# Performance work log

Hardware: AMD Instinct MI355X
Metric: run time of the kernel (lower is better)

The kernel has to match this reference:

```python
import jax, jax.numpy as jnp
import numpy as np

VOCAB, EMBED, HIDDEN = 128, 128, 256
BATCH, SEQ = 512, 512


def setup_inputs() -> dict:
    key = jax.random.key(0)
    ks = jax.random.split(key, 9)
    x = jax.random.randint(ks[0], (BATCH, SEQ), 0, VOCAB, dtype=jnp.int32)
    emb = jax.random.normal(ks[1], (VOCAB, EMBED), dtype=jnp.float32)
    s_hh = 1.0 / np.sqrt(HIDDEN)
    s_xh = 1.0 / np.sqrt(EMBED)
    s_hy = 1.0 / np.sqrt(HIDDEN)
    W_hh = jax.random.uniform(ks[2], (HIDDEN, HIDDEN), jnp.float32, -s_hh, s_hh)
    b_hh = jax.random.uniform(ks[3], (HIDDEN,), jnp.float32, -s_hh, s_hh)
    W_xh = jax.random.uniform(ks[4], (HIDDEN, EMBED), jnp.float32, -s_xh, s_xh)
    b_xh = jax.random.uniform(ks[5], (HIDDEN,), jnp.float32, -s_xh, s_xh)
    W_hy = jax.random.uniform(ks[6], (VOCAB, HIDDEN), jnp.float32, -s_hy, s_hy)
    b_hy = jax.random.uniform(ks[7], (VOCAB,), jnp.float32, -s_hy, s_hy)
    h0 = jax.random.normal(ks[8], (HIDDEN,), dtype=jnp.float32)
    return {"x": x, "emb": emb, "W_hh": W_hh, "b_hh": b_hh,
            "W_xh": W_xh, "b_xh": b_xh, "W_hy": W_hy, "b_hy": b_hy, "h0": h0}


def reference(x, emb, W_hh, b_hh, W_xh, b_xh, W_hy, b_hy, h0):
    xe = emb[x]                      # [B, S, E]
    B, S, E = xe.shape
    x0 = xe[:, 0]                    # first-token embedding, added every step (quirk in source)
    h_init = jnp.broadcast_to(h0, (B, h0.shape[0]))  # learned initial hidden, broadcast over batch

    def step(h, xt):
        h = jnp.tanh(h @ W_hh.T + b_hh + (xt + x0) @ W_xh.T + b_xh)
        y = h @ W_hy.T + b_hy        # [B, vocab]
        return h, y

    xs = jnp.swapaxes(xe[:, : S - 1], 0, 1)  # [S-1, B, E]
    _, ys = jax.lax.scan(step, h_init, xs)   # ys: [S-1, B, vocab]
    return jnp.swapaxes(ys, 0, 1)            # [B, S-1, vocab]
```

## Files before the change

kernel.cpp:

```cpp
#include <hip/hip_runtime.h>
#include <math.h>

namespace {
constexpr int SEQ   = 512;
constexpr int VOCAB = 128;
constexpr int EMBED = 128;
constexpr int HID   = 256;
constexpr int NSTEP = 511;
constexpr int BLK   = 512;
constexpr int NROW  = 2;
constexpr int NBLK  = 256;
}

__device__ float g_P[VOCAB * HID];

__global__ void precompute_P(const float* __restrict__ emb,
                             const float* __restrict__ Wxh)
{
    __shared__ __align__(16) float es[EMBED];
    const int v = blockIdx.x;
    const int j = threadIdx.x;
    if (j < EMBED) es[j] = emb[(size_t)v * EMBED + j];
    __syncthreads();
    const float4* w4 = (const float4*)(Wxh + (size_t)j * EMBED);
    const float4* e4 = (const float4*)es;
    float a = 0.f;
    #pragma unroll
    for (int k = 0; k < EMBED / 4; ++k) {
        float4 w = w4[k], e = e4[k];
        a += w.x * e.x + w.y * e.y + w.z * e.z + w.w * e.w;
    }
    g_P[v * HID + j] = a;
}

__device__ __forceinline__ int swz_c(int c) { return c ^ ((c >> 3) & 7); }

template<int WSTAG>
__global__ __launch_bounds__(BLK, 2)
void rnn_fused3(const int* __restrict__ x,   const float* __restrict__ Whh,
                const float* __restrict__ bhh, const float* __restrict__ bxh,
                const float* __restrict__ Why, const float* __restrict__ bhy,
                const float* __restrict__ h0,  float* __restrict__ out)
{
    __shared__ __align__(16) float h_s[2 * NROW * HID];

    const int tid = threadIdx.x;
    const int r0  = blockIdx.x * NROW;

    const int lk  = tid & 7;
    const int jg  = tid >> 3;
    const int jsel = (jg << 2) | (tid & 3);
    const int rsel = (tid & 4) ? 1 : 0;
    const int v0  = jg << 1;

    float whh[4][32];
    #pragma unroll
    for (int jj = 0; jj < 4; ++jj) {
        const float4* s4 = (const float4*)(Whh + (size_t)((jg << 2) + jj) * HID + (lk << 5));
        #pragma unroll
        for (int k4 = 0; k4 < 8; ++k4) {
            float4 f = s4[k4];
            whh[jj][4*k4+0] = f.x; whh[jj][4*k4+1] = f.y;
            whh[jj][4*k4+2] = f.z; whh[jj][4*k4+3] = f.w;
        }
    }
    float wy[2][32];
    #pragma unroll
    for (int r = 0; r < 2; ++r) {
        const float4* s4 = (const float4*)(Why + (size_t)(v0 + r) * HID + (lk << 5));
        #pragma unroll
        for (int k4 = 0; k4 < 8; ++k4) {
            float4 f = s4[k4];
            wy[r][4*k4+0] = f.x; wy[r][4*k4+1] = f.y;
            wy[r][4*k4+2] = f.z; wy[r][4*k4+3] = f.w;
        }
    }

    int hoff[8];
    #pragma unroll
    for (int i = 0; i < 8; ++i) hoff[i] = (lk << 7) + ((i ^ lk) << 4);

    int hwoff;
    {
        int c = jsel >> 2;
        hwoff = ((tid & 4) << 6) + ((swz_c(c) << 2) | (jsel & 3));
    }

    {
        int row = tid >> 8, j = tid & 255;
        h_s[row * HID + ((swz_c(j >> 2) << 2) | (j & 3))] = h0[j];
    }

    const size_t xb0 = (size_t)r0 * SEQ;
    const size_t xb1 = xb0 + SEQ;
    const int i00 = x[xb0];
    const int i01 = x[xb1];
    const int i0sel = rsel ? i01 : i00;
    const float pinit = g_P[(size_t)i0sel * HID + jsel];
    const float cst   = pinit + bhh[jsel] + bxh[jsel];
    float pt = pinit;
    int inx0 = x[xb0 + 1];
    int inx1 = x[xb1 + 1];

    const int orow = (lk >> 1) & 1;
    const int ov   = v0 + (lk & 1);
    float* outp = out + (size_t)(r0 + orow) * NSTEP * VOCAB + ov;
    const float bsel = bhy[ov];

    __syncthreads();

    for (int t = 0; t < NSTEP; ++t) {
        const int cur = t & 1, nxt = cur ^ 1;

        const int isel = rsel ? inx1 : inx0;
        const float pn = g_P[(size_t)isel * HID + jsel];
        {
            int tt = t + 2; tt = (tt < SEQ) ? tt : (SEQ - 1);
            inx0 = x[xb0 + tt];
            inx1 = x[xb1 + tt];
        }

        const char* hpar = (const char*)h_s + (cur << 11);
        float a0[4] = {0,0,0,0};
        float a1[4] = {0,0,0,0};
        #pragma unroll
        for (int i = 0; i < 8; ++i) {
            float4 h0v = *(const float4*)(hpar + hoff[i]);
            float4 h1v = *(const float4*)(hpar + 1024 + hoff[i]);
            #pragma unroll
            for (int jj = 0; jj < 4; ++jj) {
                a0[jj] += whh[jj][4*i+0]*h0v.x + whh[jj][4*i+1]*h0v.y
                        + whh[jj][4*i+2]*h0v.z + whh[jj][4*i+3]*h0v.w;
                a1[jj] += whh[jj][4*i+0]*h1v.x + whh[jj][4*i+1]*h1v.y
                        + whh[jj][4*i+2]*h1v.z + whh[jj][4*i+3]*h1v.w;
            }
        }
        float u0, u1;
        {
            float k0 = (lk & 1) ? a0[1] : a0[0];
            float s0 = (lk & 1) ? a0[0] : a0[1];
            k0 += __shfl_xor(s0, 1);
            float k1 = (lk & 1) ? a0[3] : a0[2];
            float s1 = (lk & 1) ? a0[2] : a0[3];
            k1 += __shfl_xor(s1, 1);
            float ka = (lk & 2) ? k1 : k0;
            float sa = (lk & 2) ? k0 : k1;
            ka += __shfl_xor(sa, 2);
            ka += __shfl_xor(ka, 4);
            u0 = ka;
        }
        {
            float k0 = (lk & 1) ? a1[1] : a1[0];
            float s0 = (lk & 1) ? a1[0] : a1[1];
            k0 += __shfl_xor(s0, 1);
            float k1 = (lk & 1) ? a1[3] : a1[2];
            float s1 = (lk & 1) ? a1[2] : a1[3];
            k1 += __shfl_xor(s1, 1);
            float ka = (lk & 2) ? k1 : k0;
            float sa = (lk & 2) ? k0 : k1;
            ka += __shfl_xor(sa, 2);
            ka += __shfl_xor(ka, 4);
            u1 = ka;
        }
        {
            float u = (rsel ? u1 : u0) + cst + pt;
            float e = __expf(2.0f * u);
            float hn = 1.0f - 2.0f / (e + 1.0f);
            h_s[(nxt << 9) + hwoff] = hn;
        }
        pt = pn;

        __syncthreads();

        {
            const char* hp = (const char*)h_s + (nxt << 11);
            float b00 = 0.f, b10 = 0.f, b01 = 0.f, b11 = 0.f;
            #pragma unroll
            for (int i = 0; i < 8; ++i) {
                float4 h0v = *(const float4*)(hp + hoff[i]);
                float4 h1v = *(const float4*)(hp + 1024 + hoff[i]);
                b00 += wy[0][4*i+0]*h0v.x + wy[0][4*i+1]*h0v.y
                     + wy[0][4*i+2]*h0v.z + wy[0][4*i+3]*h0v.w;
                b10 += wy[1][4*i+0]*h0v.x + wy[1][4*i+1]*h0v.y
                     + wy[1][4*i+2]*h0v.z + wy[1][4*i+3]*h0v.w;
                b01 += wy[0][4*i+0]*h1v.x + wy[0][4*i+1]*h1v.y
                     + wy[0][4*i+2]*h1v.z + wy[0][4*i+3]*h1v.w;
                b11 += wy[1][4*i+0]*h1v.x + wy[1][4*i+1]*h1v.y
                     + wy[1][4*i+2]*h1v.z + wy[1][4*i+3]*h1v.w;
            }
            float kr0 = (lk & 1) ? b10 : b00;
            float sr0 = (lk & 1) ? b00 : b10;
            kr0 += __shfl_xor(sr0, 1);
            float kr1 = (lk & 1) ? b11 : b01;
            float sr1 = (lk & 1) ? b01 : b11;
            kr1 += __shfl_xor(sr1, 1);
            float kv = (lk & 2) ? kr1 : kr0;
            float sv = (lk & 2) ? kr0 : kr1;
            kv += __shfl_xor(sv, 2);
            kv += __shfl_xor(kv, 4);
            if (lk < 4) *outp = kv + bsel;
            outp += VOCAB;
        }
    }
}

extern "C" void kernel_launch(void* const* d_in, const int* in_sizes, int n_in,
                              void* d_out, int out_size, void* d_ws, size_t ws_size,
                              hipStream_t stream)
{
    (void)in_sizes; (void)n_in; (void)d_ws; (void)out_size;
    const int*   x   = (const int*)  d_in[0];
    const float* emb = (const float*)d_in[1];
    const float* Whh = (const float*)d_in[2];
    const float* bhh = (const float*)d_in[3];
    const float* Wxh = (const float*)d_in[4];
    const float* bxh = (const float*)d_in[5];
    const float* Why = (const float*)d_in[6];
    const float* bhy = (const float*)d_in[7];
    const float* h0  = (const float*)d_in[8];
    float* out = (float*)d_out;

    precompute_P<<<VOCAB, 256, 0, stream>>>(emb, Wxh);

    const size_t needH  = (size_t)512 * 511 * 256 * 4;
    const size_t needHU = 2 * needH;
    if (ws_size >= needHU) {
        rnn_fused3<2><<<NBLK, BLK, 0, stream>>>(x, Whh, bhh, bxh, Why, bhy, h0, out);
    } else if (ws_size >= needH) {
        rnn_fused3<1><<<NBLK, BLK, 0, stream>>>(x, Whh, bhh, bxh, Why, bhy, h0, out);
    } else {
        rnn_fused3<0><<<NBLK, BLK, 0, stream>>>(x, Whh, bhh, bxh, Why, bhy, h0, out);
    }
}
```

Baseline: 1.076 ms.

## Move recurrent and output matmuls onto fp16 MFMA with hi/lo split

Replaces the scalar FP32 recurrence with MFMA 16x16x32 fp16 instructions. Each block now handles 16 batch rows with 4 waves instead of 2 rows with 512 threads. Both weights and hidden state are split into fp16 hi and lo parts, and three MFMAs per tile keep near-FP32 accuracy for the recurrent matmul. The output projection uses only the hi parts. Occupancy drops to 32 blocks on the device, and some precision is lost in the output projection, in exchange for far fewer FLOP instructions per step and fewer shuffle reductions.

```diff
diff --git a/kernel.cpp b/kernel.cpp
--- a/kernel.cpp
+++ b/kernel.cpp
@@ -1,5 +1,8 @@
 #include <hip/hip_runtime.h>
 #include <math.h>
+
+typedef _Float16 f16x8 __attribute__((ext_vector_type(8)));
+typedef float    f32x4 __attribute__((ext_vector_type(4)));
 
 namespace {
 constexpr int SEQ   = 512;
@@ -7,9 +10,11 @@
 constexpr int EMBED = 128;
 constexpr int HID   = 256;
 constexpr int NSTEP = 511;
-constexpr int BLK   = 512;
-constexpr int NROW  = 2;
-constexpr int NBLK  = 256;
+constexpr int BLK   = 256;
+constexpr int NROW  = 16;
+constexpr int NBLK  = 32;
+constexpr int NTA   = 4;
+constexpr int NTB   = 2;
 }
 
 __device__ float g_P[VOCAB * HID];
@@ -33,174 +38,170 @@
     g_P[v * HID + j] = a;
 }
 
-__device__ __forceinline__ int swz_c(int c) { return c ^ ((c >> 3) & 7); }
-
-template<int WSTAG>
-__global__ __launch_bounds__(BLK, 2)
-void rnn_fused3(const int* __restrict__ x,   const float* __restrict__ Whh,
-                const float* __restrict__ bhh, const float* __restrict__ bxh,
-                const float* __restrict__ Why, const float* __restrict__ bhy,
-                const float* __restrict__ h0,  float* __restrict__ out)
-{
-    __shared__ __align__(16) float h_s[2 * NROW * HID];
-
-    const int tid = threadIdx.x;
-    const int r0  = blockIdx.x * NROW;
-
-    const int lk  = tid & 7;
-    const int jg  = tid >> 3;
-    const int jsel = (jg << 2) | (tid & 3);
-    const int rsel = (tid & 4) ? 1 : 0;
-    const int v0  = jg << 1;
-
-    float whh[4][32];
-    #pragma unroll
-    for (int jj = 0; jj < 4; ++jj) {
-        const float4* s4 = (const float4*)(Whh + (size_t)((jg << 2) + jj) * HID + (lk << 5));
-        #pragma unroll
-        for (int k4 = 0; k4 < 8; ++k4) {
-            float4 f = s4[k4];
-            whh[jj][4*k4+0] = f.x; whh[jj][4*k4+1] = f.y;
-            whh[jj][4*k4+2] = f.z; whh[jj][4*k4+3] = f.w;
-        }
-    }
-    float wy[2][32];
-    #pragma unroll
-    for (int r = 0; r < 2; ++r) {
-        const float4* s4 = (const float4*)(Why + (size_t)(v0 + r) * HID + (lk << 5));
-        #pragma unroll
-        for (int k4 = 0; k4 < 8; ++k4) {
-            float4 f = s4[k4];
-            wy[r][4*k4+0] = f.x; wy[r][4*k4+1] = f.y;
-            wy[r][4*k4+2] = f.z; wy[r][4*k4+3] = f.w;
-        }
-    }
-
-    int hoff[8];
-    #pragma unroll
-    for (int i = 0; i < 8; ++i) hoff[i] = (lk << 7) + ((i ^ lk) << 4);
-
-    int hwoff;
+__device__ __forceinline__ void load_hilo(const float* s, f16x8& h8, f16x8& l8)
+{
+    float4 A = *(const float4*)s, B = *(const float4*)(s + 4);
+    _Float16 h;
+    h = (_Float16)A.x; h8[0] = h; l8[0] = (_Float16)(A.x - (float)h);
+    h = (_Float16)A.y; h8[1] = h; l8[1] = (_Float16)(A.y - (float)h);
+    h = (_Float16)A.z; h8[2] = h; l8[2] = (_Float16)(A.z - (float)h);
+    h = (_Float16)A.w; h8[3] = h; l8[3] = (_Float16)(A.w - (float)h);
+    h = (_Float16)B.x; h8[4] = h; l8[4] = (_Float16)(B.x - (float)h);
+    h = (_Float16)B.y; h8[5] = h; l8[5] = (_Float16)(B.y - (float)h);
+    h = (_Float16)B.z; h8[6] = h; l8[6] = (_Float16)(B.z - (float)h);
+    h = (_Float16)B.w; h8[7] = h; l8[7] = (_Float16)(B.w - (float)h);
+}
+
+
+__global__ __launch_bounds__(BLK, 1)
+void rnn_mfma5(const int* __restrict__ x,   const float* __restrict__ Whh,
+               const float* __restrict__ bhh, const float* __restrict__ bxh,
+               const float* __restrict__ Why, const float* __restrict__ bhy,
+               const float* __restrict__ h0,  float* __restrict__ out)
+{
+    __shared__ __align__(16) _Float16 hbuf_hi[2][NROW][HID];
+    __shared__ __align__(16) _Float16 hbuf_lo[2][NROW][HID];
+
+    const int tid  = threadIdx.x;
+    const int w    = tid >> 6;
+    const int lane = tid & 63;
+    const int ll   = lane & 15;
+    const int lh   = lane >> 4;
+    const int r0   = blockIdx.x * NROW;
+
+    f16x8 wa_hi[NTA][8], wa_lo[NTA][8];
+    #pragma unroll
+    for (int a = 0; a < NTA; ++a)
+        #pragma unroll
+        for (int f = 0; f < 8; ++f)
+            load_hilo(Whh + (size_t)(64 * w + 16 * a + ll) * HID + 32 * f + 8 * lh,
+                      wa_hi[a][f], wa_lo[a][f]);
+    f16x8 wy_hi[NTB][8];
+    #pragma unroll
+    for (int b = 0; b < NTB; ++b)
+        #pragma unroll
+        for (int f = 0; f < 8; ++f) {
+            f16x8 dummy_lo;
+            load_hilo(Why + (size_t)(32 * w + 16 * b + ll) * HID + 32 * f + 8 * lh,
+                      wy_hi[b][f], dummy_lo);
+        }
+
     {
-        int c = jsel >> 2;
-        hwoff = ((tid & 4) << 6) + ((swz_c(c) << 2) | (jsel & 3));
-    }
-
-    {
-        int row = tid >> 8, j = tid & 255;
-        h_s[row * HID + ((swz_c(j >> 2) << 2) | (j & 3))] = h0[j];
-    }
-
-    const size_t xb0 = (size_t)r0 * SEQ;
-    const size_t xb1 = xb0 + SEQ;
-    const int i00 = x[xb0];
-    const int i01 = x[xb1];
-    const int i0sel = rsel ? i01 : i00;
-    const float pinit = g_P[(size_t)i0sel * HID + jsel];
-    const float cst   = pinit + bhh[jsel] + bxh[jsel];
-    float pt = pinit;
-    int inx0 = x[xb0 + 1];
-    int inx1 = x[xb1 + 1];
-
-    const int orow = (lk >> 1) & 1;
-    const int ov   = v0 + (lk & 1);
-    float* outp = out + (size_t)(r0 + orow) * NSTEP * VOCAB + ov;
-    const float bsel = bhy[ov];
+        int k = tid;
+        float v = h0[k];
+        _Float16 hi = (_Float16)v;
+        _Float16 lo = (_Float16)(v - (float)hi);
+        int g = k >> 3, bb = k & 7;
+        #pragma unroll
+        for (int m = 0; m < NROW; ++m) {
+            int e = ((g ^ (m & 7)) << 3) + bb;
+            hbuf_hi[1][m][e] = hi;
+            hbuf_lo[1][m][e] = lo;
+        }
+    }
+
+    float cst[NTA][4], pt[NTA][4];
+    int   inx[4];
+    #pragma unroll
+    for (int r = 0; r < 4; ++r) {
+        const size_t xrow = (size_t)(r0 + 4 * lh + r) * SEQ;
+        int i0 = x[xrow];
+        #pragma unroll
+        for (int a = 0; a < NTA; ++a) {
+            int j = 64 * w + 16 * a + ll;
+            float p = g_P[(size_t)i0 * HID + j];
+            pt[a][r]  = p;
+            cst[a][r] = p + bhh[j] + bxh[j];
+        }
+        inx[r] = x[xrow + 1];
+    }
+    float bv[NTB];
+    #pragma unroll
+    for (int b = 0; b < NTB; ++b) bv[b] = bhy[32 * w + 16 * b + ll];
+
+    int aoff[8];
+    #pragma unroll
+    for (int f = 0; f < 8; ++f)
+        aoff[f] = 512 * ll + ((((f << 2) + lh) ^ (ll & 7)) << 4);
 
     __syncthreads();
 
+    f16x8 af_hi[8], af_lo[8];
+    #pragma unroll
+    for (int f = 0; f < 8; ++f) {
+        af_hi[f] = *(const f16x8*)((const char*)&hbuf_hi[1][0][0] + aoff[f]);
+        af_lo[f] = *(const f16x8*)((const char*)&hbuf_lo[1][0][0] + aoff[f]);
+    }
+
     for (int t = 0; t < NSTEP; ++t) {
-        const int cur = t & 1, nxt = cur ^ 1;
-
-        const int isel = rsel ? inx1 : inx0;
-        const float pn = g_P[(size_t)isel * HID + jsel];
+        f32x4 acc_hh[NTA] = {{0,0,0,0},{0,0,0,0},{0,0,0,0},{0,0,0,0}};
+        f32x4 acc_cr[NTA] = {{0,0,0,0},{0,0,0,0},{0,0,0,0},{0,0,0,0}};
+        #pragma unroll
+        for (int f = 0; f < 8; ++f) {
+            #pragma unroll
+            for (int a = 0; a < NTA; ++a)
+                acc_hh[a] = __builtin_amdgcn_mfma_f32_16x16x32_f16(af_hi[f], wa_hi[a][f], acc_hh[a], 0, 0, 0);
+            #pragma unroll
+            for (int a = 0; a < NTA; ++a)
+                acc_cr[a] = __builtin_amdgcn_mfma_f32_16x16x32_f16(af_lo[f], wa_hi[a][f], acc_cr[a], 0, 0, 0);
+            #pragma unroll
+            for (int a = 0; a < NTA; ++a)
+                acc_cr[a] = __builtin_amdgcn_mfma_f32_16x16x32_f16(af_hi[f], wa_lo[a][f], acc_cr[a], 0, 0, 0);
+        }
+
+        char* whi = (char*)&hbuf_hi[t & 1][0][0];
+        char* wlo = (char*)&hbuf_lo[t & 1][0][0];
+        #pragma unroll
+        for (int a = 0; a < NTA; ++a) {
+            #pragma unroll
+            for (int r = 0; r < 4; ++r) {
+                float u = (acc_hh[a][r] + acc_cr[a][r]) + cst[a][r] + pt[a][r];
+                float e  = __expf(2.0f * u);
+                float hv = 1.0f - 2.0f / (e + 1.0f);
+                _Float16 hi = (_Float16)hv;
+                _Float16 lo = (_Float16)(hv - (float)hi);
+                int m = 4 * lh + r;
+                int j = 64 * w + 16 * a + ll;
+                int off = 512 * m + ((((j >> 3)) ^ (m & 7)) << 4) + ((j & 7) << 1);
+                *(_Float16*)(whi + off) = hi;
+                *(_Float16*)(wlo + off) = lo;
+            }
+        }
+
+        #pragma unroll
+        for (int r = 0; r < 4; ++r)
+            #pragma unroll
+            for (int a = 0; a < NTA; ++a)
+                pt[a][r] = g_P[(size_t)inx[r] * HID + 64 * w + 16 * a + ll];
         {
-            int tt = t + 2; tt = (tt < SEQ) ? tt : (SEQ - 1);
-            inx0 = x[xb0 + tt];
-            inx1 = x[xb1 + tt];
-        }
-
-        const char* hpar = (const char*)h_s + (cur << 11);
-        float a0[4] = {0,0,0,0};
-        float a1[4] = {0,0,0,0};
-        #pragma unroll
-        for (int i = 0; i < 8; ++i) {
-            float4 h0v = *(const float4*)(hpar + hoff[i]);
-            float4 h1v = *(const float4*)(hpar + 1024 + hoff[i]);
-            #pragma unroll
-            for (int jj = 0; jj < 4; ++jj) {
-                a0[jj] += whh[jj][4*i+0]*h0v.x + whh[jj][4*i+1]*h0v.y
-                        + whh[jj][4*i+2]*h0v.z + whh[jj][4*i+3]*h0v.w;
-                a1[jj] += whh[jj][4*i+0]*h1v.x + whh[jj][4*i+1]*h1v.y
-                        + whh[jj][4*i+2]*h1v.z + whh[jj][4*i+3]*h1v.w;
-            }
-        }
-        float u0, u1;
-        {
-            float k0 = (lk & 1) ? a0[1] : a0[0];
-            float s0 = (lk & 1) ? a0[0] : a0[1];
-            k0 += __shfl_xor(s0, 1);
-            float k1 = (lk & 1) ? a0[3] : a0[2];
-            float s1 = (lk & 1) ? a0[2] : a0[3];
-            k1 += __shfl_xor(s1, 1);
-            float ka = (lk & 2) ? k1 : k0;
-            float sa = (lk & 2) ? k0 : k1;
-            ka += __shfl_xor(sa, 2);
-            ka += __shfl_xor(ka, 4);
-            u0 = ka;
-        }
-        {
-            float k0 = (lk & 1) ? a1[1] : a1[0];
-            float s0 = (lk & 1) ? a1[0] : a1[1];
-            k0 += __shfl_xor(s0, 1);
-            float k1 = (lk & 1) ? a1[3] : a1[2];
-            float s1 = (lk & 1) ? a1[2] : a1[3];
-            k1 += __shfl_xor(s1, 1);
-            float ka = (lk & 2) ? k1 : k0;
-            float sa = (lk & 2) ? k0 : k1;
-            ka += __shfl_xor(sa, 2);
-            ka += __shfl_xor(ka, 4);
-            u1 = ka;
-        }
-        {
-            float u = (rsel ? u1 : u0) + cst + pt;
-            float e = __expf(2.0f * u);
-            float hn = 1.0f - 2.0f / (e + 1.0f);
-            h_s[(nxt << 9) + hwoff] = hn;
-        }
-        pt = pn;
+            int tt = (t + 2 < SEQ) ? t + 2 : SEQ - 1;
+            #pragma unroll
+            for (int r = 0; r < 4; ++r)
+                inx[r] = x[(size_t)(r0 + 4 * lh + r) * SEQ + tt];
+        }
 
         __syncthreads();
 
-        {
-            const char* hp = (const char*)h_s + (nxt << 11);
-            float b00 = 0.f, b10 = 0.f, b01 = 0.f, b11 = 0.f;
-            #pragma unroll
-            for (int i = 0; i < 8; ++i) {
-                float4 h0v = *(const float4*)(hp + hoff[i]);
-                float4 h1v = *(const float4*)(hp + 1024 + hoff[i]);
-                b00 += wy[0][4*i+0]*h0v.x + wy[0][4*i+1]*h0v.y
-                     + wy[0][4*i+2]*h0v.z + wy[0][4*i+3]*h0v.w;
-                b10 += wy[1][4*i+0]*h0v.x + wy[1][4*i+1]*h0v.y
-                     + wy[1][4*i+2]*h0v.z + wy[1][4*i+3]*h0v.w;
-                b01 += wy[0][4*i+0]*h1v.x + wy[0][4*i+1]*h1v.y
-                     + wy[0][4*i+2]*h1v.z + wy[0][4*i+3]*h1v.w;
-                b11 += wy[1][4*i+0]*h1v.x + wy[1][4*i+1]*h1v.y
-                     + wy[1][4*i+2]*h1v.z + wy[1][4*i+3]*h1v.w;
-            }
-            float kr0 = (lk & 1) ? b10 : b00;
-            float sr0 = (lk & 1) ? b00 : b10;
-            kr0 += __shfl_xor(sr0, 1);
-            float kr1 = (lk & 1) ? b11 : b01;
-            float sr1 = (lk & 1) ? b01 : b11;
-            kr1 += __shfl_xor(sr1, 1);
-            float kv = (lk & 2) ? kr1 : kr0;
-            float sv = (lk & 2) ? kr0 : kr1;
-            kv += __shfl_xor(sv, 2);
-            kv += __shfl_xor(kv, 4);
-            if (lk < 4) *outp = kv + bsel;
-            outp += VOCAB;
-        }
+        const char* rhi = (const char*)&hbuf_hi[t & 1][0][0];
+        const char* rlo = (const char*)&hbuf_lo[t & 1][0][0];
+        #pragma unroll
+        for (int f = 0; f < 8; ++f) {
+            af_hi[f] = *(const f16x8*)(rhi + aoff[f]);
+            af_lo[f] = *(const f16x8*)(rlo + aoff[f]);
+        }
+
+        f32x4 yb[NTB] = {{0,0,0,0},{0,0,0,0}};
+        #pragma unroll
+        for (int f = 0; f < 8; ++f)
+            #pragma unroll
+            for (int b = 0; b < NTB; ++b)
+                yb[b] = __builtin_amdgcn_mfma_f32_16x16x32_f16(af_hi[f], wy_hi[b][f], yb[b], 0, 0, 0);
+        #pragma unroll
+        for (int b = 0; b < NTB; ++b)
+            #pragma unroll
+            for (int r = 0; r < 4; ++r)
+                out[((size_t)(r0 + 4 * lh + r) * NSTEP + t) * VOCAB + 32 * w + 16 * b + ll]
+                    = yb[b][r] + bv[b];
     }
 }
 
@@ -208,7 +209,7 @@
                               void* d_out, int out_size, void* d_ws, size_t ws_size,
                               hipStream_t stream)
 {
-    (void)in_sizes; (void)n_in; (void)d_ws; (void)out_size;
+    (void)in_sizes; (void)n_in; (void)d_ws; (void)ws_size; (void)out_size;
     const int*   x   = (const int*)  d_in[0];
     const float* emb = (const float*)d_in[1];
     const float* Whh = (const float*)d_in[2];
@@ -221,14 +222,5 @@
     float* out = (float*)d_out;
 
     precompute_P<<<VOCAB, 256, 0, stream>>>(emb, Wxh);
-
-    const size_t needH  = (size_t)512 * 511 * 256 * 4;
-    const size_t needHU = 2 * needH;
-    if (ws_size >= needHU) {
-        rnn_fused3<2><<<NBLK, BLK, 0, stream>>>(x, Whh, bhh, bxh, Why, bhy, h0, out);
-    } else if (ws_size >= needH) {
-        rnn_fused3<1><<<NBLK, BLK, 0, stream>>>(x, Whh, bhh, bxh, Why, bhy, h0, out);
-    } else {
-        rnn_fused3<0><<<NBLK, BLK, 0, stream>>>(x, Whh, bhh, bxh, Why, bhy, h0, out);
-    }
-}
+    rnn_mfma5<<<NBLK, BLK, 0, stream>>>(x, Whh, bhh, bxh, Why, bhy, h0, out);
+}
```

Result: slower. 1.363 ms (+26.7%).
